# Performance work log

Measured on AMD Instinct MI355X. Metric: run time of the kernel, lower is better.

Reference implementation:

```python
import jax, jax.numpy as jnp
import numpy as np

H = 512      # hidden size
V = 10000    # input_output_size (vocab)
L = 32       # max_length
B = 256      # batch
SOS = 1


def setup_inputs() -> dict:
    key = jax.random.key(0)
    ks = jax.random.split(key, 20)
    g = lambda k, shape: jax.random.normal(k, shape, dtype=jnp.float32) * 0.05
    return dict(
        input_tensor=jax.random.randint(ks[0], (B, L), 0, V),
        target_tensor=jax.random.randint(ks[1], (B, L), 0, V),
        # encoder: embedding + GRU
        enc_embed=g(ks[2], (V, H)),
        enc_w_ih=g(ks[3], (3 * H, H)), enc_w_hh=g(ks[4], (3 * H, H)),
        enc_b_ih=g(ks[5], (3 * H,)), enc_b_hh=g(ks[6], (3 * H,)),
        # attention decoder: embedding + attn + attn_combine + GRU + out
        dec_embed=g(ks[7], (V, H)),
        attn_w=g(ks[8], (L, 2 * H)), attn_b=g(ks[9], (L,)),
        comb_w=g(ks[10], (H, 2 * H)), comb_b=g(ks[11], (H,)),
        dec_w_ih=g(ks[12], (3 * H, H)), dec_w_hh=g(ks[13], (3 * H, H)),
        dec_b_ih=g(ks[14], (3 * H,)), dec_b_hh=g(ks[15], (3 * H,)),
        out_w=g(ks[16], (V, H)), out_b=g(ks[17], (V,)),
    )


def _gru_step(x, h, w_ih, w_hh, b_ih, b_hh):
    # PyTorch GRUCell math. x, h: [B, H]
    gi = x @ w_ih.T + b_ih          # [B, 3H]
    gh = h @ w_hh.T + b_hh          # [B, 3H]
    i_r, i_z, i_n = jnp.split(gi, 3, axis=-1)
    h_r, h_z, h_n = jnp.split(gh, 3, axis=-1)
    r = jax.nn.sigmoid(i_r + h_r)
    z = jax.nn.sigmoid(i_z + h_z)
    n = jnp.tanh(i_n + r * h_n)
    return (1.0 - z) * n + z * h


def reference(input_tensor, target_tensor,
              enc_embed, enc_w_ih, enc_w_hh, enc_b_ih, enc_b_hh,
              dec_embed, attn_w, attn_b, comb_w, comb_b,
              dec_w_ih, dec_w_hh, dec_b_ih, dec_b_hh, out_w, out_b):
    inp_t = input_tensor.T   # [L, B]
    tgt_t = target_tensor.T  # [L, B]
    h0 = jnp.zeros((B, H), dtype=enc_embed.dtype)

    # ---- encoder: scan over time ----
    def enc_step(h, tok):
        x = enc_embed[tok]  # [B, H]
        h2 = _gru_step(x, h, enc_w_ih, enc_w_hh, enc_b_ih, enc_b_hh)
        return h2, h2       # encoder output == hidden

    enc_hidden, enc_outs = jax.lax.scan(enc_step, h0, inp_t)  # enc_outs: [L, B, H]

    # ---- decoder with teacher forcing (phase='train', ratio=1.0) ----
    sos = jnp.full((1, B), SOS, dtype=tgt_t.dtype)
    dec_inputs = jnp.concatenate([sos, tgt_t[:-1]], axis=0)  # [L, B]

    def dec_step(h, tok):
        emb = dec_embed[tok]                                   # [B, H]
        aw = jax.nn.softmax(jnp.concatenate([emb, h], axis=-1) @ attn_w.T + attn_b)  # [B, L]
        applied = jnp.einsum('bl,lbh->bh', aw, enc_outs)       # attention over encoder outputs
        x = jax.nn.relu(jnp.concatenate([emb, applied], axis=-1) @ comb_w.T + comb_b)
        h2 = _gru_step(x, h, dec_w_ih, dec_w_hh, dec_b_ih, dec_b_hh)
        logits = jax.nn.log_softmax(h2 @ out_w.T + out_b)      # [B, V]
        return h2, logits

    _, network_outputs = jax.lax.scan(dec_step, enc_hidden, dec_inputs)  # [L, B, V]
    return network_outputs
```

## Files before the change

kernel.cpp:

```cpp
#include <hip/hip_runtime.h>

#define HD 512
#define VOC 10000
#define SL 32
#define BA 256
#define BH (BA*HD)

typedef __bf16 b16x8 __attribute__((ext_vector_type(8)));
typedef float f32x4 __attribute__((ext_vector_type(4)));
typedef unsigned u32x4 __attribute__((ext_vector_type(4)));

__device__ __forceinline__ ushort f2bf(float x) {
  unsigned u = __float_as_uint(x);
  u += 0x7fffu + ((u >> 16) & 1u);
  return (ushort)(u >> 16);
}

__device__ __forceinline__ void stg_sc(void* p, u32x4 v) {
  asm volatile("global_store_dwordx4 %0, %1, off sc0 sc1"
               :: "v"(p), "v"(v) : "memory");
}
__device__ __forceinline__ void stg_sc1(void* p, unsigned v) {
  asm volatile("global_store_dword %0, %1, off sc0 sc1"
               :: "v"(p), "v"(v) : "memory");
}
__device__ __forceinline__ void stg_plain(void* p, unsigned v) {
  asm volatile("global_store_dword %0, %1, off"
               :: "v"(p), "v"(v) : "memory");
}
__device__ __forceinline__ unsigned ldg_sc0(const void* p) {
  unsigned v;
  asm volatile("global_load_dword %0, %1, off sc0"
               : "=v"(v) : "v"(p) : "memory");
  asm volatile("s_waitcnt vmcnt(0)" ::: "memory");
  return v;
}
__device__ __forceinline__ unsigned ldg_sc1(const void* p) {
  unsigned v;
  asm volatile("global_load_dword %0, %1, off sc0 sc1"
               : "=v"(v) : "v"(p) : "memory");
  asm volatile("s_waitcnt vmcnt(0)" ::: "memory");
  return v;
}
__device__ __forceinline__ void vmwait0() {
  asm volatile("s_waitcnt vmcnt(0)" ::: "memory");
  __builtin_amdgcn_sched_barrier(0);
}

__global__ __launch_bounds__(256) void cvt_k(const float* __restrict__ in,
                                             ushort* __restrict__ out, int n4) {
  int i = blockIdx.x * 256 + threadIdx.x;
  if (i < n4) {
    float4 v = ((const float4*)in)[i];
    ((ushort4*)out)[i] = make_ushort4(f2bf(v.x), f2bf(v.y), f2bf(v.z), f2bf(v.w));
  }
}

__global__ __launch_bounds__(64) void gather_enc_k(const float* __restrict__ table,
                                                   const int* __restrict__ toks,
                                                   ushort* __restrict__ out) {
  int row = blockIdx.x;
  int l = row >> 8, b = row & 255;
  int tok = toks[b * SL + l];
  const float4* src = (const float4*)(table + (size_t)tok * HD);
  int t = threadIdx.x;
  float4 v0 = src[t * 2], v1 = src[t * 2 + 1];
  uint4 o;
  o.x = (unsigned)f2bf(v0.x) | ((unsigned)f2bf(v0.y) << 16);
  o.y = (unsigned)f2bf(v0.z) | ((unsigned)f2bf(v0.w) << 16);
  o.z = (unsigned)f2bf(v1.x) | ((unsigned)f2bf(v1.y) << 16);
  o.w = (unsigned)f2bf(v1.z) | ((unsigned)f2bf(v1.w) << 16);
  *(uint4*)(out + (size_t)row * HD + t * 8) = o;
}

__global__ __launch_bounds__(64) void gather_dec_k(const float* __restrict__ table,
                                                   const int* __restrict__ toks,
                                                   ushort* __restrict__ out) {
  int row = blockIdx.x;
  int l = row >> 8, b = row & 255;
  int tok = (l == 0) ? 1 : toks[b * SL + l - 1];
  const float4* src = (const float4*)(table + (size_t)tok * HD);
  int t = threadIdx.x;
  float4 v0 = src[t * 2], v1 = src[t * 2 + 1];
  uint4 o;
  o.x = (unsigned)f2bf(v0.x) | ((unsigned)f2bf(v0.y) << 16);
  o.y = (unsigned)f2bf(v0.z) | ((unsigned)f2bf(v0.w) << 16);
  o.z = (unsigned)f2bf(v1.x) | ((unsigned)f2bf(v1.y) << 16);
  o.w = (unsigned)f2bf(v1.z) | ((unsigned)f2bf(v1.w) << 16);
  *(uint4*)(out + (size_t)row * HD + t * 8) = o;
}

__global__ __launch_bounds__(256) void gemm_k(
    const ushort* __restrict__ A, const ushort* __restrict__ W,
    int N, int ldw, const float* __restrict__ bias,
    float* __restrict__ outf, int ldc) {
  __shared__ ushort lsA[4][64][8];
  __shared__ ushort lsB[4][64][8];
  __shared__ float ctile[64][68];
  int t = threadIdx.x;
  int lane = t & 63, w = t >> 6;
  int m0 = blockIdx.x * 64, n0 = blockIdx.y * 64;
  f32x4 acc[4] = {};
  int sr = t >> 2, g = t & 3;
  const ushort* Ap = A + (size_t)(m0 + sr) * HD + g * 8;
  int nr = n0 + sr; if (nr > N - 1) nr = N - 1;
  const ushort* Wp = W + (size_t)nr * ldw + g * 8;
  for (int ks = 0; ks < 16; ++ks) {
    *(uint4*)(&lsA[g][sr][0]) = *(const uint4*)(Ap + ks * 32);
    *(uint4*)(&lsB[g][sr][0]) = *(const uint4*)(Wp + ks * 32);
    __syncthreads();
    int gg = lane >> 4, r = lane & 15;
    b16x8 bf = *(const b16x8*)(&lsB[gg][w * 16 + r][0]);
#pragma unroll
    for (int mi = 0; mi < 4; ++mi) {
      b16x8 af = *(const b16x8*)(&lsA[gg][mi * 16 + r][0]);
      acc[mi] = __builtin_amdgcn_mfma_f32_16x16x32_bf16(af, bf, acc[mi], 0, 0, 0);
    }
    __syncthreads();
  }
  int gg = lane >> 4, cl = lane & 15;
  int tcol = w * 16 + cl;
  int bc = n0 + tcol; if (bc > N - 1) bc = N - 1;
  float bv = bias ? bias[bc] : 0.f;
#pragma unroll
  for (int mi = 0; mi < 4; ++mi)
#pragma unroll
    for (int r = 0; r < 4; ++r)
      ctile[mi * 16 + gg * 4 + r][tcol] = acc[mi][r] + bv;
  __syncthreads();
  int row = t >> 2, q = t & 3;
#pragma unroll
  for (int j = 0; j < 4; ++j) {
    int c = q * 16 + j * 4;
    if (n0 + c + 3 <= N - 1)
      *(float4*)(outf + (size_t)(m0 + row) * ldc + n0 + c) =
          *(const float4*)&ctile[row][c];
  }
}

__global__ __launch_bounds__(256) void gemm128_k(
    const ushort* __restrict__ A, const ushort* __restrict__ W,
    int N, const float* __restrict__ bias,
    float* __restrict__ outf, int ldc) {
  __shared__ ushort lsA[4][128][8];
  __shared__ ushort lsB[4][64][8];
  __shared__ float ctile[128][68];
  int t = threadIdx.x, lane = t & 63, w = t >> 6;
  int m0 = blockIdx.x * 128, n0 = blockIdx.y * 64;
  f32x4 acc[8] = {};
  int arow = t >> 1, ag = t & 1;
  const ushort* Ap = A + (size_t)(m0 + arow) * HD + ag * 16;
  int brow = t >> 2, bg = t & 3;
  int nr = n0 + brow; if (nr > N - 1) nr = N - 1;
  const ushort* Wp = W + (size_t)nr * HD + bg * 8;
  for (int ks = 0; ks < 16; ++ks) {
    *(uint4*)(&lsA[ag * 2][arow][0])     = *(const uint4*)(Ap + ks * 32);
    *(uint4*)(&lsA[ag * 2 + 1][arow][0]) = *(const uint4*)(Ap + ks * 32 + 8);
    *(uint4*)(&lsB[bg][brow][0])         = *(const uint4*)(Wp + ks * 32);
    __syncthreads();
    int gg = lane >> 4, r = lane & 15;
    b16x8 bf = *(const b16x8*)(&lsB[gg][w * 16 + r][0]);
#pragma unroll
    for (int mi = 0; mi < 8; ++mi) {
      b16x8 af = *(const b16x8*)(&lsA[gg][mi * 16 + r][0]);
      acc[mi] = __builtin_amdgcn_mfma_f32_16x16x32_bf16(af, bf, acc[mi], 0, 0, 0);
    }
    __syncthreads();
  }
  int gg = lane >> 4, cl = lane & 15;
  int tcol = w * 16 + cl;
  int bc = n0 + tcol; if (bc > N - 1) bc = N - 1;
  float bv = bias[bc];
#pragma unroll
  for (int mi = 0; mi < 8; ++mi)
#pragma unroll
    for (int r = 0; r < 4; ++r)
      ctile[mi * 16 + gg * 4 + r][tcol] = acc[mi][r] + bv;
  __syncthreads();
  int row = t >> 1, hf = t & 1;
#pragma unroll
  for (int j = 0; j < 8; ++j) {
    int c = hf * 32 + j * 4;
    if (n0 + c + 3 <= N - 1)
      *(float4*)(outf + (size_t)(m0 + row) * ldc + n0 + c) =
          *(const float4*)&ctile[row][c];
  }
}


union ScrU {
  float red[2][6][64][4];
  struct { float sS[2][32][33]; float sAW[32][33]; } at;
};

struct CoopArgs {
  const ushort* enc_emb_bf;
  ushort* enc_outs_bf;
  ushort* H2_bf;
  ushort* H2_rm;
  ushort* x_bf;
  ushort* applied_bf;
  const ushort* enc_wih; const ushort* enc_whh;
  const float* enc_b_ih; const float* enc_b_hh;
  const ushort* dec_wih; const ushort* dec_whh;
  const float* dec_b_ih; const float* dec_b_hh;
  const ushort* attn_w_bf;
  const float* attn_pre;
  const ushort* comb_w_bf;
  const float* comb_pre;
  unsigned* fL2;
  unsigned* fLLC;
};

__device__ __forceinline__ const ushort* sfrag(const ushort* base, int kh,
                                               int gg, int row) {
  return base + (kh * 16 + (gg >> 1)) * 4096 + row * 16 + (gg & 1) * 8;
}

template <bool XS>
__device__ __forceinline__ void gru_phase(
    int r0, int sl, int lane, int w, int t,
    const ushort* __restrict__ x_src, const ushort* __restrict__ h_src,
    const ushort (*Wlds)[2][8][64][8],
    const float* __restrict__ b_ih, const float* __restrict__ b_hh,
    float* hp, ushort* __restrict__ hbf_dst, ushort* __restrict__ hrm_dst,
    float (*red)[6][64][4], ushort (*stile)[16]) {
  int mf = w & 1, kh = w >> 1;
  int lr = lane & 15, gg = lane >> 4;
  int row_a = r0 + mf * 16 + lr;
  b16x8 xa[8], ha[8];
  if (XS) {
    const ushort* xr = sfrag(x_src, kh, gg, row_a);
#pragma unroll
    for (int ks = 0; ks < 8; ++ks) xa[ks] = *(const b16x8*)(xr + ks * 8192);
  } else {
    const ushort* xr = x_src + (size_t)row_a * HD + kh * 256 + gg * 8;
#pragma unroll
    for (int ks = 0; ks < 8; ++ks) xa[ks] = *(const b16x8*)(xr + ks * 32);
  }
  if (h_src) {
    const ushort* hr = sfrag(h_src, kh, gg, row_a);
#pragma unroll
    for (int ks = 0; ks < 8; ++ks) ha[ks] = *(const b16x8*)(hr + ks * 8192);
  } else {
#pragma unroll
    for (int ks = 0; ks < 8; ++ks) ha[ks] = b16x8{};
  }
  f32x4 acc[6] = {};
#pragma unroll
  for (int ks = 0; ks < 8; ++ks) {
#pragma unroll
    for (int g3 = 0; g3 < 3; ++g3) {
      b16x8 bi = *(const b16x8*)(&Wlds[g3][kh][ks][lane][0]);
      b16x8 bh = *(const b16x8*)(&Wlds[3 + g3][kh][ks][lane][0]);
      acc[g3] = __builtin_amdgcn_mfma_f32_16x16x32_bf16(xa[ks], bi, acc[g3], 0, 0, 0);
      acc[3 + g3] = __builtin_amdgcn_mfma_f32_16x16x32_bf16(ha[ks], bh, acc[3 + g3], 0, 0, 0);
    }
  }
  if (kh == 1) {
#pragma unroll
    for (int s = 0; s < 6; ++s) *(f32x4*)&red[mf][s][lane][0] = acc[s];
  }
  __syncthreads();
  if (kh == 0) {
    int j = sl * 16 + lr;
#pragma unroll
    for (int s = 0; s < 6; ++s) acc[s] += *(const f32x4*)&red[mf][s][lane][0];
    float bir = b_ih[j], biz = b_ih[512 + j], bin_ = b_ih[1024 + j];
    float bhr = b_hh[j], bhz = b_hh[512 + j], bhn = b_hh[1024 + j];
#pragma unroll
    for (int ri = 0; ri < 4; ++ri) {
      float ir = acc[0][ri] + bir, iz = acc[1][ri] + biz, inn = acc[2][ri] + bin_;
      float hr2 = acc[3][ri] + bhr, hz = acc[4][ri] + bhz, hn = acc[5][ri] + bhn;
      float rr = 1.f / (1.f + expf(-(ir + hr2)));
      float zz = 1.f / (1.f + expf(-(iz + hz)));
      float nn = tanhf(inn + rr * hn);
      float h2 = (1.f - zz) * nn + zz * hp[ri];
      hp[ri] = h2;
      stile[mf * 16 + gg * 4 + ri][lr] = f2bf(h2);
    }
  }
  __syncthreads();
  if (t < 64) {
    stg_sc(hbf_dst + sl * 4096 + r0 * 16 + t * 8, ((const u32x4*)stile)[t]);
    if (hrm_dst) {
      int row = t >> 1, c = t & 1;
      *(uint4*)(hrm_dst + (size_t)(r0 + row) * HD + sl * 16 + c * 8) =
          *(const uint4*)&stile[row][c * 8];
    }
  }
}

__device__ __forceinline__ void comb_phase(
    int r0, int sl, int lane, int w, int t, int l,
    const ushort* __restrict__ applied,
    const ushort (*Clds)[8][64][8],
    const float* __restrict__ comb_pre, ushort* __restrict__ x_dst,
    float (*red)[6][64][4], ushort (*stile)[16]) {
  int mf = w & 1, kh = w >> 1;
  int lr = lane & 15, gg = lane >> 4;
  int row_a = r0 + mf * 16 + lr;
  const ushort* ar = sfrag(applied, kh, gg, row_a);
  f32x4 acc = {};
#pragma unroll
  for (int ks = 0; ks < 8; ++ks) {
    b16x8 av = *(const b16x8*)(ar + ks * 8192);
    b16x8 bv = *(const b16x8*)(&Clds[kh][ks][lane][0]);
    acc = __builtin_amdgcn_mfma_f32_16x16x32_bf16(av, bv, acc, 0, 0, 0);
  }
  if (kh == 1) *(f32x4*)&red[mf][0][lane][0] = acc;
  __syncthreads();
  if (kh == 0) {
    acc += *(const f32x4*)&red[mf][0][lane][0];
    int n = sl * 16 + lr;
#pragma unroll
    for (int ri = 0; ri < 4; ++ri) {
      int row = r0 + mf * 16 + gg * 4 + ri;
      float v = acc[ri] + comb_pre[((size_t)l * BA + row) * HD + n];
      v = fmaxf(v, 0.f);
      stile[mf * 16 + gg * 4 + ri][lr] = f2bf(v);
    }
  }
  __syncthreads();
  if (t < 64)
    stg_sc(x_dst + sl * 4096 + r0 * 16 + t * 8, ((const u32x4*)stile)[t]);
}

__device__ __forceinline__ void attn_phase(
    int r0, int sl, int lane, int w, int t, int l,
    const ushort* __restrict__ h_bf,
    const ushort* __restrict__ attn_w_bf,
    const float* __restrict__ attn_pre, const ushort* __restrict__ enc_bf,
    ushort* __restrict__ applied_dst,
    float (*sS)[32][33], float (*sAW)[33], ushort (*stile)[16]) {
  int mf = w & 1, kh = w >> 1;
  int lr = lane & 15, gg = lane >> 4;
  int row_a = r0 + mf * 16 + lr;
  const ushort* hr = sfrag(h_bf, kh, gg, row_a);
  const ushort* w0 = attn_w_bf + (size_t)lr * 1024 + 512 + kh * 256 + gg * 8;
  const ushort* w1 = attn_w_bf + (size_t)(16 + lr) * 1024 + 512 + kh * 256 + gg * 8;
  f32x4 a0 = {}, a1 = {};
#pragma unroll
  for (int ks = 0; ks < 8; ++ks) {
    b16x8 ah = *(const b16x8*)(hr + ks * 8192);
    b16x8 b0 = *(const b16x8*)(w0 + ks * 32);
    b16x8 b1 = *(const b16x8*)(w1 + ks * 32);
    a0 = __builtin_amdgcn_mfma_f32_16x16x32_bf16(ah, b0, a0, 0, 0, 0);
    a1 = __builtin_amdgcn_mfma_f32_16x16x32_bf16(ah, b1, a1, 0, 0, 0);
  }
#pragma unroll
  for (int ri = 0; ri < 4; ++ri) {
    sS[kh][mf * 16 + gg * 4 + ri][lr] = a0[ri];
    sS[kh][mf * 16 + gg * 4 + ri][16 + lr] = a1[ri];
  }
  __syncthreads();
  int r = t >> 3, q = t & 7;
  float4 pre = *(const float4*)(attn_pre + ((size_t)l * BA + r0 + r) * 32 + q * 4);
  float v0 = sS[0][r][q * 4 + 0] + sS[1][r][q * 4 + 0] + pre.x;
  float v1 = sS[0][r][q * 4 + 1] + sS[1][r][q * 4 + 1] + pre.y;
  float v2 = sS[0][r][q * 4 + 2] + sS[1][r][q * 4 + 2] + pre.z;
  float v3 = sS[0][r][q * 4 + 3] + sS[1][r][q * 4 + 3] + pre.w;
  float mx = fmaxf(fmaxf(v0, v1), fmaxf(v2, v3));
  for (int o = 1; o < 8; o <<= 1) mx = fmaxf(mx, __shfl_xor(mx, o, 64));
  float e0 = expf(v0 - mx), e1 = expf(v1 - mx), e2 = expf(v2 - mx), e3 = expf(v3 - mx);
  float s = e0 + e1 + e2 + e3;
  for (int o = 1; o < 8; o <<= 1) s += __shfl_xor(s, o, 64);
  float inv = 1.f / s;
  sAW[r][q * 4 + 0] = e0 * inv; sAW[r][q * 4 + 1] = e1 * inv;
  sAW[r][q * 4 + 2] = e2 * inv; sAW[r][q * 4 + 3] = e3 * inv;
  __syncthreads();
  int rr = t >> 3, dp = t & 7;
  float f0 = 0.f, f1 = 0.f;
  const ushort* ep = enc_bf + sl * 4096 + (r0 + rr) * 16 + dp * 2;
#pragma unroll 8
  for (int ll = 0; ll < 32; ++ll) {
    float aw = sAW[rr][ll];
    unsigned u = *(const unsigned*)(ep + (size_t)ll * BH);
    f0 += aw * __uint_as_float(u << 16);
    f1 += aw * __uint_as_float(u & 0xffff0000u);
  }
  unsigned ov = (unsigned)f2bf(f0) | ((unsigned)f2bf(f1) << 16);
  *(unsigned*)&stile[rr][dp * 2] = ov;
  __syncthreads();
  if (t < 64)
    stg_sc(applied_dst + sl * 4096 + r0 * 16 + t * 8, ((const u32x4*)stile)[t]);
}

__global__ __launch_bounds__(256) void coop_k(CoopArgs a) {
  __shared__ ushort Wlds[6][2][8][64][8];
  __shared__ ushort Clds[2][8][64][8];
  __shared__ ScrU scr;
  __shared__ ushort stile[32][16];
  int bid = blockIdx.x;
  int rg = bid & 7, sl = bid >> 3;
  int t = threadIdx.x, lane = t & 63, w = t >> 6;
  int r0 = rg * 32;
  unsigned* fL2 = a.fL2 + rg * 32 * 4;
  unsigned* fLLC = a.fLLC + rg * 32 * 16;
  unsigned sync_idx = 0;

  auto gsync = [&]() {
    ++sync_idx;
    __syncthreads();
    if (w == 0) {
      vmwait0();
      if (lane == 0) {
        stg_plain(&fL2[sl * 4], sync_idx);
        stg_sc1(&fLLC[sl * 16], sync_idx);
      }
      int it = 0;
      for (;;) {
        unsigned v = ldg_sc0(&fL2[(lane & 31) * 4]);
        if (!__any(v < sync_idx)) break;
        if ((++it & 3) == 0) {
          unsigned v2 = ldg_sc1(&fLLC[(lane & 31) * 16]);
          if (!__any(v < sync_idx && v2 < sync_idx)) break;
        }
        __builtin_amdgcn_s_sleep(1);
      }
    }
    __syncthreads();
  };

  auto load_gru_w = [&](const ushort* Wih, const ushort* Whh) {
    for (int c = w; c < 96; c += 4) {
      int g = c >> 4, rem = c & 15, kh2 = rem >> 3, ks = rem & 7;
      const ushort* src = (g < 3) ? Wih : Whh;
      int gr = (g % 3) * 512 + sl * 16 + (lane & 15);
      int col = kh2 * 256 + ks * 32 + (lane >> 4) * 8;
      *(uint4*)&Wlds[g][kh2][ks][lane][0] =
          *(const uint4*)(src + (size_t)gr * HD + col);
    }
  };

  load_gru_w(a.enc_wih, a.enc_whh);
  __syncthreads();

  float hp[4] = {0.f, 0.f, 0.f, 0.f};

  for (int l = 0; l < SL; ++l) {
    gru_phase<false>(r0, sl, lane, w, t,
                     a.enc_emb_bf + (size_t)l * BH,
                     l ? a.enc_outs_bf + (size_t)(l - 1) * BH : nullptr,
                     Wlds, a.enc_b_ih, a.enc_b_hh,
                     hp, a.enc_outs_bf + (size_t)l * BH, nullptr,
                     scr.red, stile);
    gsync();
  }

  load_gru_w(a.dec_wih, a.dec_whh);
  for (int c = w; c < 16; c += 4) {
    int kh2 = c >> 3, ks = c & 7;
    int gr = sl * 16 + (lane & 15);
    int col = 512 + kh2 * 256 + ks * 32 + (lane >> 4) * 8;
    *(uint4*)&Clds[kh2][ks][lane][0] =
        *(const uint4*)(a.comb_w_bf + (size_t)gr * 1024 + col);
  }
  __syncthreads();

  for (int l = 0; l < SL; ++l) {
    const ushort* h_bf = l ? a.H2_bf + (size_t)(l - 1) * BH
                           : a.enc_outs_bf + (size_t)31 * BH;
    attn_phase(r0, sl, lane, w, t, l, h_bf, a.attn_w_bf, a.attn_pre,
               a.enc_outs_bf, a.applied_bf + (size_t)l * BH,
               scr.at.sS, scr.at.sAW, stile);
    gsync();
    comb_phase(r0, sl, lane, w, t, l, a.applied_bf + (size_t)l * BH,
               Clds, a.comb_pre, a.x_bf + (size_t)l * BH, scr.red, stile);
    gsync();
    gru_phase<true>(r0, sl, lane, w, t, a.x_bf + (size_t)l * BH, h_bf,
                    Wlds, a.dec_b_ih, a.dec_b_hh,
                    hp, a.H2_bf + (size_t)l * BH,
                    a.H2_rm + (size_t)l * BH, scr.red, stile);
    gsync();
  }
}

__global__ __launch_bounds__(256) void lsesub_k(float* __restrict__ logits) {
  __shared__ float redm[4], reds[4];
  int row = blockIdx.x, t = threadIdx.x;
  float4* p = (float4*)(logits + (size_t)row * VOC);
  float4 v[10];
  float m = -1e30f, s = 0.f;
#pragma unroll
  for (int j = 0; j < 10; ++j) {
    int i = t + j * 256;
    if (i < 2500) {
      v[j] = p[i];
      float mx = fmaxf(fmaxf(v[j].x, v[j].y), fmaxf(v[j].z, v[j].w));
      if (mx > m) { s *= expf(m - mx); m = mx; }
      s += expf(v[j].x - m) + expf(v[j].y - m) + expf(v[j].z - m) + expf(v[j].w - m);
    }
  }
#pragma unroll
  for (int o = 32; o; o >>= 1) {
    float m2 = __shfl_xor(m, o, 64), s2 = __shfl_xor(s, o, 64);
    float mn = fmaxf(m, m2);
    s = s * expf(m - mn) + s2 * expf(m2 - mn);
    m = mn;
  }
  if ((t & 63) == 0) { redm[t >> 6] = m; reds[t >> 6] = s; }
  __syncthreads();
  float mf = fmaxf(fmaxf(redm[0], redm[1]), fmaxf(redm[2], redm[3]));
  float sf = reds[0] * expf(redm[0] - mf) + reds[1] * expf(redm[1] - mf) +
             reds[2] * expf(redm[2] - mf) + reds[3] * expf(redm[3] - mf);
  float z = mf + logf(sf);
#pragma unroll
  for (int j = 0; j < 10; ++j) {
    int i = t + j * 256;
    if (i < 2500) {
      v[j].x -= z; v[j].y -= z; v[j].z -= z; v[j].w -= z;
      p[i] = v[j];
    }
  }
}

extern "C" void kernel_launch(void* const* d_in, const int* in_sizes, int n_in,
                              void* d_out, int out_size, void* d_ws, size_t ws_size,
                              hipStream_t stream) {
  (void)in_sizes; (void)n_in; (void)out_size; (void)ws_size;
  const int* in_tok = (const int*)d_in[0];
  const int* tgt_tok = (const int*)d_in[1];
  const float* enc_embed = (const float*)d_in[2];
  const float* enc_w_ih = (const float*)d_in[3];
  const float* enc_w_hh = (const float*)d_in[4];
  const float* enc_b_ih = (const float*)d_in[5];
  const float* enc_b_hh = (const float*)d_in[6];
  const float* dec_embed = (const float*)d_in[7];
  const float* attn_w = (const float*)d_in[8];
  const float* attn_b = (const float*)d_in[9];
  const float* comb_w = (const float*)d_in[10];
  const float* comb_b = (const float*)d_in[11];
  const float* dec_w_ih = (const float*)d_in[12];
  const float* dec_w_hh = (const float*)d_in[13];
  const float* dec_b_ih = (const float*)d_in[14];
  const float* dec_b_hh = (const float*)d_in[15];
  const float* out_w = (const float*)d_in[16];
  const float* out_b = (const float*)d_in[17];
  float* out = (float*)d_out;

  char* ws = (char*)d_ws;
  size_t off = 0;
  auto carve = [&](size_t bytes) {
    void* p = ws + off;
    off += (bytes + 255) & ~(size_t)255;
    return p;
  };
  ushort* enc_wih_bf = (ushort*)carve(1536 * 512 * 2);
  ushort* enc_whh_bf = (ushort*)carve(1536 * 512 * 2);
  ushort* dec_wih_bf = (ushort*)carve(1536 * 512 * 2);
  ushort* dec_whh_bf = (ushort*)carve(1536 * 512 * 2);
  ushort* comb_w_bf  = (ushort*)carve(512 * 1024 * 2);
  ushort* attn_w_bf  = (ushort*)carve(32 * 1024 * 2);
  ushort* out_w_bf   = (ushort*)carve((size_t)VOC * HD * 2);
  ushort* enc_emb_bf = (ushort*)carve((size_t)SL * BA * HD * 2);
  ushort* dec_emb_bf = (ushort*)carve((size_t)SL * BA * HD * 2);
  float* attn_pre    = (float*)carve((size_t)SL * BA * 32 * 4);
  float* comb_pre    = (float*)carve((size_t)SL * BA * HD * 4);
  ushort* enc_outs_bf= (ushort*)carve((size_t)SL * BA * HD * 2);
  ushort* H2_bf      = (ushort*)carve((size_t)SL * BA * HD * 2);
  ushort* H2_rm      = (ushort*)carve((size_t)SL * BA * HD * 2);
  ushort* applied_bf = (ushort*)carve((size_t)SL * BA * HD * 2);
  ushort* x_bf       = (ushort*)carve((size_t)SL * BA * HD * 2);
  unsigned* fL2      = (unsigned*)carve(8 * 32 * 4 * 4);
  unsigned* fLLC     = (unsigned*)carve(8 * 32 * 16 * 4);

  cvt_k<<<768, 256, 0, stream>>>(enc_w_ih, enc_wih_bf, 1536 * 512 / 4);
  cvt_k<<<768, 256, 0, stream>>>(enc_w_hh, enc_whh_bf, 1536 * 512 / 4);
  cvt_k<<<768, 256, 0, stream>>>(dec_w_ih, dec_wih_bf, 1536 * 512 / 4);
  cvt_k<<<768, 256, 0, stream>>>(dec_w_hh, dec_whh_bf, 1536 * 512 / 4);
  cvt_k<<<512, 256, 0, stream>>>(comb_w, comb_w_bf, 512 * 1024 / 4);
  cvt_k<<<32, 256, 0, stream>>>(attn_w, attn_w_bf, 32 * 1024 / 4);
  cvt_k<<<5000, 256, 0, stream>>>(out_w, out_w_bf, VOC * HD / 4);
  gather_enc_k<<<SL * BA, 64, 0, stream>>>(enc_embed, in_tok, enc_emb_bf);
  gather_dec_k<<<SL * BA, 64, 0, stream>>>(dec_embed, tgt_tok, dec_emb_bf);
  hipMemsetAsync(fL2, 0, 8 * 32 * 4 * 4, stream);
  hipMemsetAsync(fLLC, 0, 8 * 32 * 16 * 4, stream);

  gemm_k<<<dim3(128, 1), 256, 0, stream>>>(dec_emb_bf, attn_w_bf, 32, 1024,
                                           attn_b, attn_pre, 32);
  gemm_k<<<dim3(128, 8), 256, 0, stream>>>(dec_emb_bf, comb_w_bf, 512, 1024,
                                           comb_b, comb_pre, 512);

  CoopArgs ca;
  ca.enc_emb_bf = enc_emb_bf;
  ca.enc_outs_bf = enc_outs_bf;
  ca.H2_bf = H2_bf;
  ca.H2_rm = H2_rm;
  ca.x_bf = x_bf;
  ca.applied_bf = applied_bf;
  ca.enc_wih = enc_wih_bf; ca.enc_whh = enc_whh_bf;
  ca.enc_b_ih = enc_b_ih; ca.enc_b_hh = enc_b_hh;
  ca.dec_wih = dec_wih_bf; ca.dec_whh = dec_whh_bf;
  ca.dec_b_ih = dec_b_ih; ca.dec_b_hh = dec_b_hh;
  ca.attn_w_bf = attn_w_bf;
  ca.attn_pre = attn_pre;
  ca.comb_w_bf = comb_w_bf;
  ca.comb_pre = comb_pre;
  ca.fL2 = fL2;
  ca.fLLC = fLLC;
  void* kargs[] = { (void*)&ca };
  hipError_t ce = hipLaunchCooperativeKernel(coop_k, dim3(256), dim3(256),
                                             kargs, 0, stream);
  if (ce != hipSuccess) {
    coop_k<<<256, 256, 0, stream>>>(ca);
  }

  gemm128_k<<<dim3(64, 157), 256, 0, stream>>>(H2_rm, out_w_bf, VOC,
                                               out_b, out, VOC);
  lsesub_k<<<SL * BA, 256, 0, stream>>>(out);
}
```

Baseline: 948.0 us.

## Precompute comb_w times encoder outputs to drop per-step comb GEMM and grid sync

The comb linear layer distributes over the attention sum: comb_w·(Σ aw·enc) equals Σ aw·(comb_w·enc). So the encoder outputs are projected once by a batched GEMM after the encoder, and each decoder step only does the weighted sum plus ReLU. This removes the per-step comb MFMA phase and one grid-wide barrier per decoder step. The single cooperative kernel is split into separate encoder and decoder kernels, the GRU weights are converted to bf16 inside those kernels, and the small conversion and gather kernels are merged to cut launches. The cost is an extra projected-encoder buffer and a different bf16 rounding order.

```diff
diff --git a/kernel.cpp b/kernel.cpp
--- a/kernel.cpp
+++ b/kernel.cpp
@@ -47,38 +47,32 @@
   __builtin_amdgcn_sched_barrier(0);
 }
 
-__global__ __launch_bounds__(256) void cvt_k(const float* __restrict__ in,
-                                             ushort* __restrict__ out, int n4) {
-  int i = blockIdx.x * 256 + threadIdx.x;
+__global__ __launch_bounds__(256) void cvt3_k(
+    const float* __restrict__ w_out, ushort* __restrict__ o_out,
+    const float* __restrict__ w_comb, ushort* __restrict__ o_comb,
+    const float* __restrict__ w_attn, ushort* __restrict__ o_attn) {
+  int b = blockIdx.x;
+  const float* in; ushort* out; int i; int n4;
+  if (b < 5000)      { in = w_out;  out = o_out;  i = b * 256 + threadIdx.x;          n4 = 1280000; }
+  else if (b < 5512) { in = w_comb; out = o_comb; i = (b - 5000) * 256 + threadIdx.x; n4 = 131072; }
+  else               { in = w_attn; out = o_attn; i = (b - 5512) * 256 + threadIdx.x; n4 = 8192; }
   if (i < n4) {
     float4 v = ((const float4*)in)[i];
     ((ushort4*)out)[i] = make_ushort4(f2bf(v.x), f2bf(v.y), f2bf(v.z), f2bf(v.w));
   }
 }
 
-__global__ __launch_bounds__(64) void gather_enc_k(const float* __restrict__ table,
-                                                   const int* __restrict__ toks,
-                                                   ushort* __restrict__ out) {
-  int row = blockIdx.x;
+__global__ __launch_bounds__(64) void gather2_k(
+    const float* __restrict__ enc_t, const float* __restrict__ dec_t,
+    const int* __restrict__ in_tok, const int* __restrict__ tgt_tok,
+    ushort* __restrict__ enc_o, ushort* __restrict__ dec_o) {
+  int bid = blockIdx.x;
+  int isDec = bid >= SL * BA;
+  int row = isDec ? bid - SL * BA : bid;
   int l = row >> 8, b = row & 255;
-  int tok = toks[b * SL + l];
-  const float4* src = (const float4*)(table + (size_t)tok * HD);
-  int t = threadIdx.x;
-  float4 v0 = src[t * 2], v1 = src[t * 2 + 1];
-  uint4 o;
-  o.x = (unsigned)f2bf(v0.x) | ((unsigned)f2bf(v0.y) << 16);
-  o.y = (unsigned)f2bf(v0.z) | ((unsigned)f2bf(v0.w) << 16);
-  o.z = (unsigned)f2bf(v1.x) | ((unsigned)f2bf(v1.y) << 16);
-  o.w = (unsigned)f2bf(v1.z) | ((unsigned)f2bf(v1.w) << 16);
-  *(uint4*)(out + (size_t)row * HD + t * 8) = o;
-}
-
-__global__ __launch_bounds__(64) void gather_dec_k(const float* __restrict__ table,
-                                                   const int* __restrict__ toks,
-                                                   ushort* __restrict__ out) {
-  int row = blockIdx.x;
-  int l = row >> 8, b = row & 255;
-  int tok = (l == 0) ? 1 : toks[b * SL + l - 1];
+  int tok = isDec ? ((l == 0) ? 1 : tgt_tok[b * SL + l - 1]) : in_tok[b * SL + l];
+  const float* table = isDec ? dec_t : enc_t;
+  ushort* out = isDec ? dec_o : enc_o;
   const float4* src = (const float4*)(table + (size_t)tok * HD);
   int t = threadIdx.x;
   float4 v0 = src[t * 2], v1 = src[t * 2 + 1];
@@ -136,6 +130,46 @@
       *(float4*)(outf + (size_t)(m0 + row) * ldc + n0 + c) =
           *(const float4*)&ctile[row][c];
   }
+}
+
+__global__ __launch_bounds__(256) void gemmW_k(
+    const ushort* __restrict__ A, const ushort* __restrict__ W,
+    ushort* __restrict__ outS) {
+  __shared__ ushort lsA[4][64][8];
+  __shared__ ushort lsB[4][64][8];
+  __shared__ ushort ctileS[64][64];
+  int t = threadIdx.x, lane = t & 63, w = t >> 6;
+  int m0 = blockIdx.x * 64, n0 = blockIdx.y * 64;
+  f32x4 acc[4] = {};
+  int sr = t >> 2, g = t & 3;
+  const ushort* Ap = A + (size_t)(m0 + sr) * HD + g * 8;
+  const ushort* Wp = W + (size_t)(n0 + sr) * 1024 + 512 + g * 8;
+  for (int ks = 0; ks < 16; ++ks) {
+    *(uint4*)(&lsA[g][sr][0]) = *(const uint4*)(Ap + ks * 32);
+    *(uint4*)(&lsB[g][sr][0]) = *(const uint4*)(Wp + ks * 32);
+    __syncthreads();
+    int gg = lane >> 4, r = lane & 15;
+    b16x8 bf = *(const b16x8*)(&lsB[gg][w * 16 + r][0]);
+#pragma unroll
+    for (int mi = 0; mi < 4; ++mi) {
+      b16x8 af = *(const b16x8*)(&lsA[gg][mi * 16 + r][0]);
+      acc[mi] = __builtin_amdgcn_mfma_f32_16x16x32_bf16(af, bf, acc[mi], 0, 0, 0);
+    }
+    __syncthreads();
+  }
+  int gg = lane >> 4, cl = lane & 15;
+  int tcol = w * 16 + cl;
+#pragma unroll
+  for (int mi = 0; mi < 4; ++mi)
+#pragma unroll
+    for (int r = 0; r < 4; ++r)
+      ctileS[mi * 16 + gg * 4 + r][tcol] = f2bf(acc[mi][r]);
+  __syncthreads();
+  int l = m0 >> 8, b0 = m0 & 255;
+  int sl_i = t >> 6, tid = t & 63;
+  ushort* dst = outS + (((size_t)l * 32 + (n0 >> 4) + sl_i) * 256 + b0 + tid) * 16;
+  *(uint4*)dst = *(const uint4*)&ctileS[tid][sl_i * 16];
+  *(uint4*)(dst + 8) = *(const uint4*)&ctileS[tid][sl_i * 16 + 8];
 }
 
 __global__ __launch_bounds__(256) void gemm128_k(
@@ -188,30 +222,6 @@
 }
 
 
-union ScrU {
-  float red[2][6][64][4];
-  struct { float sS[2][32][33]; float sAW[32][33]; } at;
-};
-
-struct CoopArgs {
-  const ushort* enc_emb_bf;
-  ushort* enc_outs_bf;
-  ushort* H2_bf;
-  ushort* H2_rm;
-  ushort* x_bf;
-  ushort* applied_bf;
-  const ushort* enc_wih; const ushort* enc_whh;
-  const float* enc_b_ih; const float* enc_b_hh;
-  const ushort* dec_wih; const ushort* dec_whh;
-  const float* dec_b_ih; const float* dec_b_hh;
-  const ushort* attn_w_bf;
-  const float* attn_pre;
-  const ushort* comb_w_bf;
-  const float* comb_pre;
-  unsigned* fL2;
-  unsigned* fLLC;
-};
-
 __device__ __forceinline__ const ushort* sfrag(const ushort* base, int kh,
                                                int gg, int row) {
   return base + (kh * 16 + (gg >> 1)) * 4096 + row * 16 + (gg & 1) * 8;
@@ -283,55 +293,17 @@
   __syncthreads();
   if (t < 64) {
     stg_sc(hbf_dst + sl * 4096 + r0 * 16 + t * 8, ((const u32x4*)stile)[t]);
-    if (hrm_dst) {
-      int row = t >> 1, c = t & 1;
-      *(uint4*)(hrm_dst + (size_t)(r0 + row) * HD + sl * 16 + c * 8) =
-          *(const uint4*)&stile[row][c * 8];
-    }
-  }
-}
-
-__device__ __forceinline__ void comb_phase(
+    int row = t >> 1, c = t & 1;
+    *(uint4*)(hrm_dst + (size_t)(r0 + row) * HD + sl * 16 + c * 8) =
+        *(const uint4*)&stile[row][c * 8];
+  }
+}
+
+__device__ __forceinline__ void attnx_phase(
     int r0, int sl, int lane, int w, int t, int l,
-    const ushort* __restrict__ applied,
-    const ushort (*Clds)[8][64][8],
+    const ushort* __restrict__ h_bf, const ushort* __restrict__ attn_w_bf,
+    const float* __restrict__ attn_pre, const ushort* __restrict__ encW,
     const float* __restrict__ comb_pre, ushort* __restrict__ x_dst,
-    float (*red)[6][64][4], ushort (*stile)[16]) {
-  int mf = w & 1, kh = w >> 1;
-  int lr = lane & 15, gg = lane >> 4;
-  int row_a = r0 + mf * 16 + lr;
-  const ushort* ar = sfrag(applied, kh, gg, row_a);
-  f32x4 acc = {};
-#pragma unroll
-  for (int ks = 0; ks < 8; ++ks) {
-    b16x8 av = *(const b16x8*)(ar + ks * 8192);
-    b16x8 bv = *(const b16x8*)(&Clds[kh][ks][lane][0]);
-    acc = __builtin_amdgcn_mfma_f32_16x16x32_bf16(av, bv, acc, 0, 0, 0);
-  }
-  if (kh == 1) *(f32x4*)&red[mf][0][lane][0] = acc;
-  __syncthreads();
-  if (kh == 0) {
-    acc += *(const f32x4*)&red[mf][0][lane][0];
-    int n = sl * 16 + lr;
-#pragma unroll
-    for (int ri = 0; ri < 4; ++ri) {
-      int row = r0 + mf * 16 + gg * 4 + ri;
-      float v = acc[ri] + comb_pre[((size_t)l * BA + row) * HD + n];
-      v = fmaxf(v, 0.f);
-      stile[mf * 16 + gg * 4 + ri][lr] = f2bf(v);
-    }
-  }
-  __syncthreads();
-  if (t < 64)
-    stg_sc(x_dst + sl * 4096 + r0 * 16 + t * 8, ((const u32x4*)stile)[t]);
-}
-
-__device__ __forceinline__ void attn_phase(
-    int r0, int sl, int lane, int w, int t, int l,
-    const ushort* __restrict__ h_bf,
-    const ushort* __restrict__ attn_w_bf,
-    const float* __restrict__ attn_pre, const ushort* __restrict__ enc_bf,
-    ushort* __restrict__ applied_dst,
     float (*sS)[32][33], float (*sAW)[33], ushort (*stile)[16]) {
   int mf = w & 1, kh = w >> 1;
   int lr = lane & 15, gg = lane >> 4;
@@ -370,8 +342,9 @@
   sAW[r][q * 4 + 2] = e2 * inv; sAW[r][q * 4 + 3] = e3 * inv;
   __syncthreads();
   int rr = t >> 3, dp = t & 7;
-  float f0 = 0.f, f1 = 0.f;
-  const ushort* ep = enc_bf + sl * 4096 + (r0 + rr) * 16 + dp * 2;
+  const float* cp = comb_pre + ((size_t)l * BA + r0 + rr) * HD + sl * 16 + dp * 2;
+  float f0 = cp[0], f1 = cp[1];
+  const ushort* ep = encW + sl * 4096 + (r0 + rr) * 16 + dp * 2;
 #pragma unroll 8
   for (int ll = 0; ll < 32; ++ll) {
     float aw = sAW[rr][ll];
@@ -379,17 +352,85 @@
     f0 += aw * __uint_as_float(u << 16);
     f1 += aw * __uint_as_float(u & 0xffff0000u);
   }
+  f0 = fmaxf(f0, 0.f); f1 = fmaxf(f1, 0.f);
   unsigned ov = (unsigned)f2bf(f0) | ((unsigned)f2bf(f1) << 16);
   *(unsigned*)&stile[rr][dp * 2] = ov;
   __syncthreads();
   if (t < 64)
-    stg_sc(applied_dst + sl * 4096 + r0 * 16 + t * 8, ((const u32x4*)stile)[t]);
-}
-
-__global__ __launch_bounds__(256) void coop_k(CoopArgs a) {
+    stg_sc(x_dst + sl * 4096 + r0 * 16 + t * 8, ((const u32x4*)stile)[t]);
+}
+
+struct EncArgs {
+  const ushort* enc_emb_bf;
+  const float* enc_w_ih; const float* enc_w_hh;
+  const float* enc_b_ih; const float* enc_b_hh;
+  ushort* enc_outs_s;
+  ushort* enc_outs_rm;
+  float* Hc;
+  unsigned* fL2; unsigned* fLLC;
+};
+
+struct DecArgs {
+  const float* dec_w_ih; const float* dec_w_hh;
+  const float* dec_b_ih; const float* dec_b_hh;
+  const ushort* attn_w_bf;
+  const float* attn_pre;
+  const float* comb_pre;
+  const ushort* enc_outs_s;
+  const ushort* encW;
+  const float* Hc;
+  ushort* H2_s; ushort* H2_rm; ushort* x_s;
+  unsigned* fL2; unsigned* fLLC;
+};
+
+union DScr {
+  float red[2][6][64][4];
+  struct { float sS[2][32][33]; float sAW[32][33]; } at;
+};
+
+#define GSYNC_DEF(fL2p, fLLCp)                                          \
+  auto gsync = [&]() {                                                  \
+    ++sync_idx;                                                         \
+    __syncthreads();                                                    \
+    if (w == 0) {                                                       \
+      vmwait0();                                                        \
+      if (lane == 0) {                                                  \
+        stg_plain(&(fL2p)[sl * 4], sync_idx);                           \
+        stg_sc1(&(fLLCp)[sl * 16], sync_idx);                           \
+      }                                                                 \
+      int it = 0;                                                       \
+      for (;;) {                                                        \
+        unsigned v = ldg_sc0(&(fL2p)[(lane & 31) * 4]);                 \
+        if (!__any(v < sync_idx)) break;                                \
+        if ((++it & 3) == 0) {                                          \
+          unsigned v2 = ldg_sc1(&(fLLCp)[(lane & 31) * 16]);            \
+          if (!__any(v < sync_idx && v2 < sync_idx)) break;             \
+        }                                                               \
+        __builtin_amdgcn_s_sleep(1);                                    \
+      }                                                                 \
+    }                                                                   \
+    __syncthreads();                                                    \
+  }
+
+#define LOAD_GRU_W32(Wih, Whh)                                          \
+  for (int c = w; c < 96; c += 4) {                                     \
+    int g = c >> 4, rem = c & 15, kh2 = rem >> 3, ks = rem & 7;         \
+    const float* src = (g < 3) ? (Wih) : (Whh);                         \
+    int gr = (g % 3) * 512 + sl * 16 + (lane & 15);                     \
+    int col = kh2 * 256 + ks * 32 + (lane >> 4) * 8;                    \
+    const float4* s4 = (const float4*)(src + (size_t)gr * HD + col);    \
+    float4 va = s4[0], vb = s4[1];                                      \
+    uint4 o;                                                            \
+    o.x = (unsigned)f2bf(va.x) | ((unsigned)f2bf(va.y) << 16);          \
+    o.y = (unsigned)f2bf(va.z) | ((unsigned)f2bf(va.w) << 16);          \
+    o.z = (unsigned)f2bf(vb.x) | ((unsigned)f2bf(vb.y) << 16);          \
+    o.w = (unsigned)f2bf(vb.z) | ((unsigned)f2bf(vb.w) << 16);          \
+    *(uint4*)&Wlds[g][kh2][ks][lane][0] = o;                            \
+  }
+
+__global__ __launch_bounds__(256) void enc_k(EncArgs a) {
   __shared__ ushort Wlds[6][2][8][64][8];
-  __shared__ ushort Clds[2][8][64][8];
-  __shared__ ScrU scr;
+  __shared__ float red[2][6][64][4];
   __shared__ ushort stile[32][16];
   int bid = blockIdx.x;
   int rg = bid & 7, sl = bid >> 3;
@@ -398,81 +439,65 @@
   unsigned* fL2 = a.fL2 + rg * 32 * 4;
   unsigned* fLLC = a.fLLC + rg * 32 * 16;
   unsigned sync_idx = 0;
-
-  auto gsync = [&]() {
-    ++sync_idx;
-    __syncthreads();
-    if (w == 0) {
-      vmwait0();
-      if (lane == 0) {
-        stg_plain(&fL2[sl * 4], sync_idx);
-        stg_sc1(&fLLC[sl * 16], sync_idx);
-      }
-      int it = 0;
-      for (;;) {
-        unsigned v = ldg_sc0(&fL2[(lane & 31) * 4]);
-        if (!__any(v < sync_idx)) break;
-        if ((++it & 3) == 0) {
-          unsigned v2 = ldg_sc1(&fLLC[(lane & 31) * 16]);
-          if (!__any(v < sync_idx && v2 < sync_idx)) break;
-        }
-        __builtin_amdgcn_s_sleep(1);
-      }
-    }
-    __syncthreads();
-  };
-
-  auto load_gru_w = [&](const ushort* Wih, const ushort* Whh) {
-    for (int c = w; c < 96; c += 4) {
-      int g = c >> 4, rem = c & 15, kh2 = rem >> 3, ks = rem & 7;
-      const ushort* src = (g < 3) ? Wih : Whh;
-      int gr = (g % 3) * 512 + sl * 16 + (lane & 15);
-      int col = kh2 * 256 + ks * 32 + (lane >> 4) * 8;
-      *(uint4*)&Wlds[g][kh2][ks][lane][0] =
-          *(const uint4*)(src + (size_t)gr * HD + col);
-    }
-  };
-
-  load_gru_w(a.enc_wih, a.enc_whh);
+  GSYNC_DEF(fL2, fLLC);
+
+  LOAD_GRU_W32(a.enc_w_ih, a.enc_w_hh);
   __syncthreads();
 
   float hp[4] = {0.f, 0.f, 0.f, 0.f};
-
   for (int l = 0; l < SL; ++l) {
     gru_phase<false>(r0, sl, lane, w, t,
                      a.enc_emb_bf + (size_t)l * BH,
-                     l ? a.enc_outs_bf + (size_t)(l - 1) * BH : nullptr,
+                     l ? a.enc_outs_s + (size_t)(l - 1) * BH : nullptr,
                      Wlds, a.enc_b_ih, a.enc_b_hh,
-                     hp, a.enc_outs_bf + (size_t)l * BH, nullptr,
-                     scr.red, stile);
+                     hp, a.enc_outs_s + (size_t)l * BH,
+                     a.enc_outs_rm + (size_t)l * BH, red, stile);
+    if (l != SL - 1) gsync();
+  }
+  if ((w >> 1) == 0) {
+    int mf2 = w & 1, gg2 = lane >> 4, j = sl * 16 + (lane & 15);
+#pragma unroll
+    for (int ri = 0; ri < 4; ++ri)
+      a.Hc[(size_t)(r0 + mf2 * 16 + gg2 * 4 + ri) * HD + j] = hp[ri];
+  }
+}
+
+__global__ __launch_bounds__(256) void dec_k(DecArgs a) {
+  __shared__ ushort Wlds[6][2][8][64][8];
+  __shared__ DScr scr;
+  __shared__ ushort stile[32][16];
+  int bid = blockIdx.x;
+  int rg = bid & 7, sl = bid >> 3;
+  int t = threadIdx.x, lane = t & 63, w = t >> 6;
+  int r0 = rg * 32;
+  unsigned* fL2 = a.fL2 + rg * 32 * 4;
+  unsigned* fLLC = a.fLLC + rg * 32 * 16;
+  unsigned sync_idx = 0;
+  GSYNC_DEF(fL2, fLLC);
+
+  LOAD_GRU_W32(a.dec_w_ih, a.dec_w_hh);
+
+  float hp[4] = {0.f, 0.f, 0.f, 0.f};
+  if ((w >> 1) == 0) {
+    int mf2 = w & 1, gg2 = lane >> 4, j = sl * 16 + (lane & 15);
+#pragma unroll
+    for (int ri = 0; ri < 4; ++ri)
+      hp[ri] = a.Hc[(size_t)(r0 + mf2 * 16 + gg2 * 4 + ri) * HD + j];
+  }
+  __syncthreads();
+
+  for (int l = 0; l < SL; ++l) {
+    const ushort* h_bf = l ? a.H2_s + (size_t)(l - 1) * BH
+                           : a.enc_outs_s + (size_t)31 * BH;
+    attnx_phase(r0, sl, lane, w, t, l, h_bf, a.attn_w_bf, a.attn_pre,
+                a.encW, a.comb_pre, a.x_s + (size_t)l * BH,
+                scr.at.sS, scr.at.sAW, stile);
     gsync();
-  }
-
-  load_gru_w(a.dec_wih, a.dec_whh);
-  for (int c = w; c < 16; c += 4) {
-    int kh2 = c >> 3, ks = c & 7;
-    int gr = sl * 16 + (lane & 15);
-    int col = 512 + kh2 * 256 + ks * 32 + (lane >> 4) * 8;
-    *(uint4*)&Clds[kh2][ks][lane][0] =
-        *(const uint4*)(a.comb_w_bf + (size_t)gr * 1024 + col);
-  }
-  __syncthreads();
-
-  for (int l = 0; l < SL; ++l) {
-    const ushort* h_bf = l ? a.H2_bf + (size_t)(l - 1) * BH
-                           : a.enc_outs_bf + (size_t)31 * BH;
-    attn_phase(r0, sl, lane, w, t, l, h_bf, a.attn_w_bf, a.attn_pre,
-               a.enc_outs_bf, a.applied_bf + (size_t)l * BH,
-               scr.at.sS, scr.at.sAW, stile);
-    gsync();
-    comb_phase(r0, sl, lane, w, t, l, a.applied_bf + (size_t)l * BH,
-               Clds, a.comb_pre, a.x_bf + (size_t)l * BH, scr.red, stile);
-    gsync();
-    gru_phase<true>(r0, sl, lane, w, t, a.x_bf + (size_t)l * BH, h_bf,
+    gru_phase<true>(r0, sl, lane, w, t, a.x_s + (size_t)l * BH, h_bf,
                     Wlds, a.dec_b_ih, a.dec_b_hh,
-                    hp, a.H2_bf + (size_t)l * BH,
+                    hp, a.H2_s + (size_t)l * BH,
                     a.H2_rm + (size_t)l * BH, scr.red, stile);
-    gsync();
+    if (l != SL - 1) gsync();
   }
 }
 
@@ -546,10 +571,6 @@
     off += (bytes + 255) & ~(size_t)255;
     return p;
   };
-  ushort* enc_wih_bf = (ushort*)carve(1536 * 512 * 2);
-  ushort* enc_whh_bf = (ushort*)carve(1536 * 512 * 2);
-  ushort* dec_wih_bf = (ushort*)carve(1536 * 512 * 2);
-  ushort* dec_whh_bf = (ushort*)carve(1536 * 512 * 2);
   ushort* comb_w_bf  = (ushort*)carve(512 * 1024 * 2);
   ushort* attn_w_bf  = (ushort*)carve(32 * 1024 * 2);
   ushort* out_w_bf   = (ushort*)carve((size_t)VOC * HD * 2);
@@ -557,54 +578,59 @@
   ushort* dec_emb_bf = (ushort*)carve((size_t)SL * BA * HD * 2);
   float* attn_pre    = (float*)carve((size_t)SL * BA * 32 * 4);
   float* comb_pre    = (float*)carve((size_t)SL * BA * HD * 4);
-  ushort* enc_outs_bf= (ushort*)carve((size_t)SL * BA * HD * 2);
-  ushort* H2_bf      = (ushort*)carve((size_t)SL * BA * HD * 2);
+  ushort* enc_outs_s = (ushort*)carve((size_t)SL * BA * HD * 2);
+  ushort* enc_outs_rm= (ushort*)carve((size_t)SL * BA * HD * 2);
+  ushort* encW       = (ushort*)carve((size_t)SL * BA * HD * 2);
+  ushort* H2_s       = (ushort*)carve((size_t)SL * BA * HD * 2);
   ushort* H2_rm      = (ushort*)carve((size_t)SL * BA * HD * 2);
-  ushort* applied_bf = (ushort*)carve((size_t)SL * BA * HD * 2);
-  ushort* x_bf       = (ushort*)carve((size_t)SL * BA * HD * 2);
-  unsigned* fL2      = (unsigned*)carve(8 * 32 * 4 * 4);
-  unsigned* fLLC     = (unsigned*)carve(8 * 32 * 16 * 4);
-
-  cvt_k<<<768, 256, 0, stream>>>(enc_w_ih, enc_wih_bf, 1536 * 512 / 4);
-  cvt_k<<<768, 256, 0, stream>>>(enc_w_hh, enc_whh_bf, 1536 * 512 / 4);
-  cvt_k<<<768, 256, 0, stream>>>(dec_w_ih, dec_wih_bf, 1536 * 512 / 4);
-  cvt_k<<<768, 256, 0, stream>>>(dec_w_hh, dec_whh_bf, 1536 * 512 / 4);
-  cvt_k<<<512, 256, 0, stream>>>(comb_w, comb_w_bf, 512 * 1024 / 4);
-  cvt_k<<<32, 256, 0, stream>>>(attn_w, attn_w_bf, 32 * 1024 / 4);
-  cvt_k<<<5000, 256, 0, stream>>>(out_w, out_w_bf, VOC * HD / 4);
-  gather_enc_k<<<SL * BA, 64, 0, stream>>>(enc_embed, in_tok, enc_emb_bf);
-  gather_dec_k<<<SL * BA, 64, 0, stream>>>(dec_embed, tgt_tok, dec_emb_bf);
-  hipMemsetAsync(fL2, 0, 8 * 32 * 4 * 4, stream);
-  hipMemsetAsync(fLLC, 0, 8 * 32 * 16 * 4, stream);
+  ushort* x_s        = (ushort*)carve((size_t)SL * BA * HD * 2);
+  float* Hc          = (float*)carve((size_t)BA * HD * 4);
+  unsigned* fE_L2    = (unsigned*)carve(8 * 32 * 4 * 4);
+  unsigned* fE_LLC   = (unsigned*)carve(8 * 32 * 16 * 4);
+  unsigned* fD_L2    = (unsigned*)carve(8 * 32 * 4 * 4);
+  unsigned* fD_LLC   = (unsigned*)carve(8 * 32 * 16 * 4);
+
+  hipMemsetAsync(fE_L2, 0, (8 * 32 * 4 + 8 * 32 * 16) * 2 * 4, stream);
+  cvt3_k<<<5544, 256, 0, stream>>>(out_w, out_w_bf, comb_w, comb_w_bf,
+                                   attn_w, attn_w_bf);
+  gather2_k<<<2 * SL * BA, 64, 0, stream>>>(enc_embed, dec_embed, in_tok,
+                                            tgt_tok, enc_emb_bf, dec_emb_bf);
 
   gemm_k<<<dim3(128, 1), 256, 0, stream>>>(dec_emb_bf, attn_w_bf, 32, 1024,
                                            attn_b, attn_pre, 32);
   gemm_k<<<dim3(128, 8), 256, 0, stream>>>(dec_emb_bf, comb_w_bf, 512, 1024,
                                            comb_b, comb_pre, 512);
 
-  CoopArgs ca;
-  ca.enc_emb_bf = enc_emb_bf;
-  ca.enc_outs_bf = enc_outs_bf;
-  ca.H2_bf = H2_bf;
-  ca.H2_rm = H2_rm;
-  ca.x_bf = x_bf;
-  ca.applied_bf = applied_bf;
-  ca.enc_wih = enc_wih_bf; ca.enc_whh = enc_whh_bf;
-  ca.enc_b_ih = enc_b_ih; ca.enc_b_hh = enc_b_hh;
-  ca.dec_wih = dec_wih_bf; ca.dec_whh = dec_whh_bf;
-  ca.dec_b_ih = dec_b_ih; ca.dec_b_hh = dec_b_hh;
-  ca.attn_w_bf = attn_w_bf;
-  ca.attn_pre = attn_pre;
-  ca.comb_w_bf = comb_w_bf;
-  ca.comb_pre = comb_pre;
-  ca.fL2 = fL2;
-  ca.fLLC = fLLC;
-  void* kargs[] = { (void*)&ca };
-  hipError_t ce = hipLaunchCooperativeKernel(coop_k, dim3(256), dim3(256),
-                                             kargs, 0, stream);
-  if (ce != hipSuccess) {
-    coop_k<<<256, 256, 0, stream>>>(ca);
-  }
+  EncArgs ea;
+  ea.enc_emb_bf = enc_emb_bf;
+  ea.enc_w_ih = enc_w_ih; ea.enc_w_hh = enc_w_hh;
+  ea.enc_b_ih = enc_b_ih; ea.enc_b_hh = enc_b_hh;
+  ea.enc_outs_s = enc_outs_s;
+  ea.enc_outs_rm = enc_outs_rm;
+  ea.Hc = Hc;
+  ea.fL2 = fE_L2; ea.fLLC = fE_LLC;
+  void* ekargs[] = { (void*)&ea };
+  hipError_t ce = hipLaunchCooperativeKernel(enc_k, dim3(256), dim3(256),
+                                             ekargs, 0, stream);
+  if (ce != hipSuccess) enc_k<<<256, 256, 0, stream>>>(ea);
+
+  gemmW_k<<<dim3(128, 8), 256, 0, stream>>>(enc_outs_rm, comb_w_bf, encW);
+
+  DecArgs da;
+  da.dec_w_ih = dec_w_ih; da.dec_w_hh = dec_w_hh;
+  da.dec_b_ih = dec_b_ih; da.dec_b_hh = dec_b_hh;
+  da.attn_w_bf = attn_w_bf;
+  da.attn_pre = attn_pre;
+  da.comb_pre = comb_pre;
+  da.enc_outs_s = enc_outs_s;
+  da.encW = encW;
+  da.Hc = Hc;
+  da.H2_s = H2_s; da.H2_rm = H2_rm; da.x_s = x_s;
+  da.fL2 = fD_L2; da.fLLC = fD_LLC;
+  void* dkargs[] = { (void*)&da };
+  ce = hipLaunchCooperativeKernel(dec_k, dim3(256), dim3(256),
+                                  dkargs, 0, stream);
+  if (ce != hipSuccess) dec_k<<<256, 256, 0, stream>>>(da);
 
   gemm128_k<<<dim3(64, 157), 256, 0, stream>>>(H2_rm, out_w_bf, VOC,
                                                out_b, out, VOC);
```

After: 893.4 us. 1.06x faster.
